# Kernel optimization log

Hardware: AMD Instinct MI355X
Metric: run time of the kernel (lower is better)

## Reference

```python
import jax, jax.numpy as jnp
import numpy as np

NEG_SLOPE = 0.2
EPS = 1e-16

N_NODES = 10000
N_EDGES = 80000
F_IN = 128
HID = 300
H1 = 5  # first_heads
H3 = 3  # out_head
N_CLASSES = 40


def gat_conv(x, edge_index, W, att_src, att_dst, bias, heads, out_ch, concat):
    """PyG-style GATConv (v1 attention), eval mode (no dropout).

    x: [N, F_in]; edge_index: [2, E] (row 0 = source, row 1 = target),
    self-loops already included. W: [F_in, heads*out_ch];
    att_src/att_dst: [heads, out_ch].
    """
    N = x.shape[0]
    h = (x @ W).reshape(N, heads, out_ch)            # [N, H, C]
    a_src = jnp.einsum('nhc,hc->nh', h, att_src)     # [N, H]
    a_dst = jnp.einsum('nhc,hc->nh', h, att_dst)     # [N, H]
    src, dst = edge_index[0], edge_index[1]
    e = jax.nn.leaky_relu(a_src[src] + a_dst[dst], NEG_SLOPE)  # [E, H]
    # segment softmax over incoming edges of each target node
    m = jax.ops.segment_max(e, dst, num_segments=N)  # [N, H]
    ex = jnp.exp(e - m[dst])
    s = jax.ops.segment_sum(ex, dst, num_segments=N)
    alpha = ex / (s[dst] + EPS)                      # [E, H]
    msg = h[src] * alpha[:, :, None]                 # [E, H, C]
    out = jax.ops.segment_sum(msg, dst, num_segments=N)  # [N, H, C]
    if concat:
        out = out.reshape(N, heads * out_ch)
    else:
        out = out.mean(axis=1)
    return out + bias


def setup_inputs() -> dict:
    key = jax.random.key(0)
    ks = jax.random.split(key, 12)
    glorot = lambda k, shape: jax.random.normal(k, shape, jnp.float32) * np.sqrt(
        2.0 / (shape[0] + shape[-1]))
    x = jax.random.normal(ks[0], (N_NODES, F_IN), jnp.float32)
    edge_index = jax.random.randint(ks[1], (2, N_EDGES), 0, N_NODES, jnp.int64)
    return {
        'x': x,
        'edge_index': edge_index,
        'W1': glorot(ks[2], (F_IN, H1 * HID)),
        'as1': glorot(ks[3], (H1, HID)),
        'ad1': glorot(ks[4], (H1, HID)),
        'b1': jnp.zeros((H1 * HID,), jnp.float32),
        'W2': glorot(ks[5], (H1 * HID, H1 * HID)),
        'as2': glorot(ks[6], (H1, HID)),
        'ad2': glorot(ks[7], (H1, HID)),
        'b2': jnp.zeros((H1 * HID,), jnp.float32),
        'W3': glorot(ks[8], (H1 * HID, H3 * N_CLASSES)),
        'as3': glorot(ks[9], (H3, N_CLASSES)),
        'ad3': glorot(ks[10], (H3, N_CLASSES)),
        'b3': jnp.zeros((N_CLASSES,), jnp.float32),
    }


def reference(x, edge_index, W1, as1, ad1, b1, W2, as2, ad2, b2, W3, as3, ad3, b3):
    N = x.shape[0]
    # PyG GATConv adds self-loops by default
    loops = jnp.arange(N, dtype=edge_index.dtype)
    ei = jnp.concatenate([edge_index, jnp.stack([loops, loops])], axis=1)
    # dropout layers are identity in eval mode
    h = gat_conv(x, ei, W1, as1, ad1, b1, H1, HID, True)
    h = jax.nn.elu(h)
    h2 = gat_conv(h, ei, W2, as2, ad2, b2, H1, HID, True)
    h = jax.nn.elu(h + h2)
    h = gat_conv(h, ei, W3, as3, ad3, b3, H3, N_CLASSES, False)  # [N, n_cls]
    pooled = h.sum(axis=0, keepdims=True)                        # [1, n_cls]
    return (pooled, jax.nn.log_softmax(pooled, axis=1))
```

## Files before the change

kernel.cpp:

```cpp
#include <hip/hip_runtime.h>
#include <hip/hip_bf16.h>
#include <math.h>

#define NN       10000
#define F_IN     128
#define HID      300
#define H1       5
#define H3       3
#define NCLS     40
#define HC1      (H1*HID)
#define KPAD     1536
#define HS12     304
#define NL12     1520
#define HS3      48
#define NL3      144
#define LD3      160
#define NEG_SLOPE 0.2f
#define EPSV     1e-16f

typedef __attribute__((ext_vector_type(8))) short bf16x8;
typedef __attribute__((ext_vector_type(8))) unsigned short u16x8;
typedef __attribute__((ext_vector_type(4))) float f32x4;

__device__ inline unsigned short f2bf(float f) {
  unsigned int u = __builtin_bit_cast(unsigned int, f);
  unsigned int r = (u + 0x7FFFu + ((u >> 16) & 1u)) >> 16;
  return (unsigned short)r;
}
__device__ inline float bf2f(unsigned short s) {
  unsigned int u = ((unsigned int)s) << 16;
  return __builtin_bit_cast(float, u);
}

__device__ __forceinline__ void gl2lds16(const unsigned short* g, unsigned short* l) {
  __builtin_amdgcn_global_load_lds(
      (const __attribute__((address_space(1))) unsigned int*)(const void*)g,
      (__attribute__((address_space(3))) unsigned int*)(void*)l, 16, 0, 0);
}

__global__ void k_count(const int* __restrict__ ei, int* __restrict__ counts,
                        int E0, int Etot) {
  int e = blockIdx.x * 256 + threadIdx.x;
  if (e >= Etot) return;
  int dst = (e < E0) ? ei[E0 + e] : (e - E0);
  atomicAdd(&counts[dst], 1);
}

__global__ __launch_bounds__(256) void k_scan(const int* __restrict__ counts,
                                              int* __restrict__ offsets,
                                              int* __restrict__ cursor,
                                              int N, int Etot) {
  __shared__ int sh[256];
  const int CH = 40;
  int t = threadIdx.x;
  int base = t * CH;
  int s = 0;
  for (int i = 0; i < CH; i++) {
    int idx = base + i;
    if (idx < N) s += counts[idx];
  }
  sh[t] = s;
  __syncthreads();
  for (int d = 1; d < 256; d <<= 1) {
    int v = (t >= d) ? sh[t - d] : 0;
    __syncthreads();
    sh[t] += v;
    __syncthreads();
  }
  int run = sh[t] - s;
  for (int i = 0; i < CH; i++) {
    int idx = base + i;
    if (idx < N) {
      offsets[idx] = run;
      cursor[idx] = run;
      run += counts[idx];
    }
  }
  if (t == 0) offsets[N] = Etot;
}

__global__ void k_scatter(const int* __restrict__ ei, int* __restrict__ cursor,
                          int* __restrict__ csr_src, int E0, int Etot) {
  int e = blockIdx.x * 256 + threadIdx.x;
  if (e >= Etot) return;
  int src, dst;
  if (e < E0) { src = ei[e]; dst = ei[E0 + e]; }
  else        { src = dst = e - E0; }
  int pos = atomicAdd(&cursor[dst], 1);
  csr_src[pos] = src;
}

__global__ void k_cvt(const float* __restrict__ in, unsigned short* __restrict__ out,
                      int R, int C, int Cpad) {
  long long idx = (long long)blockIdx.x * 256 + threadIdx.x;
  if (idx >= (long long)R * Cpad) return;
  int r = (int)(idx / Cpad), c = (int)(idx - (long long)r * Cpad);
  out[idx] = (c < C) ? f2bf(in[(size_t)r * C + c]) : 0;
}

__global__ void k_attpad3(const float* __restrict__ as1, const float* __restrict__ ad1,
                          const float* __restrict__ as2, const float* __restrict__ ad2,
                          const float* __restrict__ as3, const float* __restrict__ ad3,
                          float* __restrict__ ps1, float* __restrict__ pd1,
                          float* __restrict__ ps2, float* __restrict__ pd2,
                          float* __restrict__ ps3, float* __restrict__ pd3) {
  int i = blockIdx.x * 256 + threadIdx.x;
  if (i < KPAD) {
    int h = i / HS12, cin = i - h * HS12;
    bool live = (h < H1) && (cin < HID);
    int o = live ? (h * HID + cin) : 0;
    ps1[i] = live ? as1[o] : 0.f;
    pd1[i] = live ? ad1[o] : 0.f;
    ps2[i] = live ? as2[o] : 0.f;
    pd2[i] = live ? ad2[o] : 0.f;
  }
  if (i < LD3) {
    int h = i / HS3, cin = i - h * HS3;
    bool live = (h < H3) && (cin < NCLS);
    ps3[i] = live ? as3[h * NCLS + cin] : 0.f;
    pd3[i] = live ? ad3[h * NCLS + cin] : 0.f;
  }
}

__global__ __launch_bounds__(256) void k_cvtT3(
    const float* __restrict__ W1, const float* __restrict__ W2,
    const float* __restrict__ W3,
    unsigned short* __restrict__ o1, unsigned short* __restrict__ o2,
    unsigned short* __restrict__ o3) {
  const float* in; unsigned short* out;
  int K, Nm, kC, kS, Kp, nC, nS, Nmp;
  if (blockIdx.z == 0) {
    in = W1; out = o1; K = F_IN; Nm = HC1; kC = F_IN; kS = F_IN; Kp = F_IN;
    nC = HID; nS = HS12; Nmp = NL12;
  } else if (blockIdx.z == 1) {
    in = W2; out = o2; K = HC1; Nm = HC1; kC = HID; kS = HS12; Kp = KPAD;
    nC = HID; nS = HS12; Nmp = NL12;
  } else {
    in = W3; out = o3; K = HC1; Nm = H3 * NCLS; kC = HID; kS = HS12; Kp = KPAD;
    nC = NCLS; nS = HS3; Nmp = NL3;
  }
  int k0 = blockIdx.y * 64, n0 = blockIdx.x * 64;
  if (k0 >= Kp || n0 >= Nmp) return;
  __shared__ float tile[64][65];
  int c = threadIdx.x & 63, r = threadIdx.x >> 6;
  for (int rr = r; rr < 64; rr += 4) {
    int kp = k0 + rr;
    int np = n0 + c;
    float v = 0.f;
    if (kp < Kp && np < Nmp) {
      int ck = kp % kS, bk = kp / kS;
      int cn = np % nS, bn_ = np / nS;
      int ko = bk * kC + ck, no = bn_ * nC + cn;
      if (ck < kC && ko < K && cn < nC && no < Nm) v = in[(size_t)ko * Nm + no];
    }
    tile[rr][c] = v;
  }
  __syncthreads();
  for (int rr = r; rr < 64; rr += 4) {
    int np = n0 + rr, kp = k0 + c;
    if (np < Nmp && kp < Kp) out[(size_t)np * Kp + kp] = f2bf(tile[c][rr]);
  }
}

#define BM 256
#define BN 128
#define BK 64

__global__ __launch_bounds__(512) void gemm_mfma(
    const unsigned short* __restrict__ A,
    const unsigned short* __restrict__ Bt,
    unsigned short* __restrict__ Cbf,
    int M, int Kpad, int Nmat, int ldc, int klen, int nT,
    float* __restrict__ Cacc) {
  __shared__ unsigned short As[BM * BK];
  __shared__ unsigned short Bs[BN * BK];
  int tid = threadIdx.x;
  int lane = tid & 63, wid = tid >> 6;
  int wm = wid >> 1, wn = wid & 1;
  int bid = blockIdx.x;
  int slot = bid & 7, idx = bid >> 3;
  int nTi = idx % nT, mg = idx / nT;
  int bm = (slot + 8 * mg) * BM, bn = nTi * BN;
  int quad = lane >> 4, l16 = lane & 15;
  int kq = quad * 8;
  int koff = blockIdx.y * klen;

  int ar0 = min(bm + 32 * wid + l16, M - 1);
  int ar1 = min(bm + 32 * wid + 16 + l16, M - 1);
  int br0 = min(bn + 16 * wid + l16, Nmat - 1);
  const unsigned short* gA0 = A + (size_t)ar0 * Kpad + kq;
  const unsigned short* gA1 = A + (size_t)ar1 * Kpad + kq;
  const unsigned short* gB0 = Bt + (size_t)br0 * Kpad + kq;
  unsigned short* lA = As + 4 * wid * 512;
  unsigned short* lB = Bs + 2 * wid * 512;

  f32x4 acc[4][4] = {};

  for (int kt = koff; kt < koff + klen; kt += BK) {
    gl2lds16(gA0 + kt,      lA);
    gl2lds16(gA0 + kt + 32, lA + 512);
    gl2lds16(gA1 + kt,      lA + 1024);
    gl2lds16(gA1 + kt + 32, lA + 1536);
    gl2lds16(gB0 + kt,      lB);
    gl2lds16(gB0 + kt + 32, lB + 512);
    __syncthreads();
#pragma unroll
    for (int kh = 0; kh < 2; kh++) {
      bf16x8 af[4], bfr[4];
#pragma unroll
      for (int i = 0; i < 4; i++) {
        af[i]  = *(const bf16x8*)(As + ((wm * 4 + i) * 2 + kh) * 512 + lane * 8);
        bfr[i] = *(const bf16x8*)(Bs + ((wn * 4 + i) * 2 + kh) * 512 + lane * 8);
      }
#pragma unroll
      for (int i = 0; i < 4; i++)
#pragma unroll
        for (int j = 0; j < 4; j++)
          acc[i][j] = __builtin_amdgcn_mfma_f32_16x16x32_bf16(af[i], bfr[j], acc[i][j], 0, 0, 0);
    }
    __syncthreads();
  }

#pragma unroll
  for (int i = 0; i < 4; i++) {
    int rowb = bm + wm * 64 + i * 16 + quad * 4;
#pragma unroll
    for (int j = 0; j < 4; j++) {
      int col = bn + wn * 64 + j * 16 + l16;
      if (col < ldc) {
        bool live = col < Nmat;
        if (Cacc) {
#pragma unroll
          for (int r = 0; r < 4; r++) {
            int row = rowb + r;
            if (live && row < M) atomicAdd(&Cacc[(size_t)row * ldc + col], acc[i][j][r]);
          }
        } else {
#pragma unroll
          for (int r = 0; r < 4; r++) {
            int row = rowb + r;
            if (row < M) Cbf[(size_t)row * ldc + col] = live ? f2bf(acc[i][j][r]) : 0;
          }
        }
      }
    }
  }
}

__global__ void k_att(unsigned short* __restrict__ hfeat, int ldh,
                      const float* __restrict__ attp_s,
                      const float* __restrict__ attp_d,
                      float* __restrict__ asrc, float* __restrict__ adst,
                      int H, int HS,
                      const float* __restrict__ Cacc, int Nlive) {
  int n = blockIdx.x, t = threadIdx.x;
  __shared__ float s_ps[8], s_pd[8];
  if (t < 8) { s_ps[t] = 0.f; s_pd[t] = 0.f; }
  __syncthreads();
  int col0 = t * 8;
  if (col0 < ldh) {
    int hj = col0 / HS;
    float ps = 0.f, pd = 0.f;
    if (Cacc) {
      const float4* p = (const float4*)(Cacc + (size_t)n * ldh + col0);
      float4 f0 = p[0], f1 = p[1];
      float fv[8] = {f0.x, f0.y, f0.z, f0.w, f1.x, f1.y, f1.z, f1.w};
      u16x8 st;
#pragma unroll
      for (int j = 0; j < 8; j++) {
        bool live = (col0 + j) < Nlive;
        float v = live ? fv[j] : 0.f;
        st[j] = live ? f2bf(v) : 0;
        ps += v * attp_s[col0 + j];
        pd += v * attp_d[col0 + j];
      }
      *(u16x8*)(hfeat + (size_t)n * ldh + col0) = st;
    } else {
      u16x8 rv = *(const u16x8*)(hfeat + (size_t)n * ldh + col0);
#pragma unroll
      for (int j = 0; j < 8; j++) {
        float v = bf2f(rv[j]);
        ps += v * attp_s[col0 + j];
        pd += v * attp_d[col0 + j];
      }
    }
    atomicAdd(&s_ps[hj], ps);
    atomicAdd(&s_pd[hj], pd);
  }
  __syncthreads();
  if (t < H) {
    asrc[(size_t)n * H + t] = s_ps[t];
    adst[(size_t)n * H + t] = s_pd[t];
  }
}

__global__ __launch_bounds__(64) void k_agg(
    const unsigned short* __restrict__ hfeat, int ldh,
    const float* __restrict__ asrc,
    const float* __restrict__ adst,
    const int* __restrict__ csr_src,
    const int* __restrict__ offsets,
    const float* __restrict__ bias,
    const unsigned short* __restrict__ prevbf,
    unsigned short* __restrict__ out_bf,
    const float* __restrict__ b3,
    float* __restrict__ h3,
    int HS, int C, int H, int mode) {
  int n = blockIdx.x;
  int t = threadIdx.x;
  int s0 = offsets[n], s1 = offsets[n + 1];

  __shared__ float s_ad[8], s_pm[64], s_pl[64], s_mx[8], s_rinv[8];
  __shared__ int s_src[64];
  __shared__ float s_alpha[64 * 8];
  __shared__ float s_out[LD3];

  if (t < 8) s_ad[t] = (t < H) ? adst[(size_t)n * H + t] : 0.f;
  __syncthreads();

  int hh = t & 7, sl = t >> 3;
  float m = -1e30f, l = 0.f;
  if (hh < H) {
    float ad = s_ad[hh];
    for (int p = s0 + sl; p < s1; p += 8) {
      float v = asrc[csr_src[p] * H + hh] + ad;
      v = v > 0.f ? v : NEG_SLOPE * v;
      if (v > m) { l = l * expf(m - v) + 1.f; m = v; }
      else       { l += expf(v - m); }
    }
  }
  s_pm[t] = m; s_pl[t] = l;
  __syncthreads();
  if (t < 8) {
    float M2 = -1e30f, L2 = 0.f;
    for (int k = 0; k < 8; k++) {
      float mk = s_pm[t + 8 * k], lk = s_pl[t + 8 * k];
      if (mk > M2) { L2 = L2 * expf(M2 - mk) + lk; M2 = mk; }
      else         { L2 += lk * expf(mk - M2); }
    }
    s_mx[t] = M2;
    s_rinv[t] = 1.f / (L2 + EPSV);
  }
  __syncthreads();

  int col0 = blockIdx.y * 512 + t * 8;
  bool active = col0 < ldh;
  int hj = active ? (col0 / HS) : 0;
  int cbase = col0 - hj * HS;
  float acc[8] = {};

  for (int base = s0; base < s1; base += 64) {
    int chunk = min(64, s1 - base);
    if (t < chunk) {
      int srcn = csr_src[base + t];
      s_src[t] = srcn;
      const float* ar = asrc + (size_t)srcn * H;
#pragma unroll
      for (int h = 0; h < 8; h++) {
        float a = 0.f;
        if (h < H) {
          float v = ar[h] + s_ad[h];
          v = v > 0.f ? v : NEG_SLOPE * v;
          a = expf(v - s_mx[h]) * s_rinv[h];
        }
        s_alpha[t * 8 + h] = a;
      }
    }
    __syncthreads();
    if (active) {
      const unsigned short* hb = hfeat + col0;
      u16x8 rv0 = {}, rv1 = {};
      if (chunk > 0) rv0 = *(const u16x8*)(hb + (size_t)s_src[0] * ldh);
      if (chunk > 1) rv1 = *(const u16x8*)(hb + (size_t)s_src[1] * ldh);
      int e = 0;
      for (; e + 2 <= chunk; e += 2) {
        u16x8 c0 = rv0, c1 = rv1;
        if (e + 2 < chunk) rv0 = *(const u16x8*)(hb + (size_t)s_src[e + 2] * ldh);
        if (e + 3 < chunk) rv1 = *(const u16x8*)(hb + (size_t)s_src[e + 3] * ldh);
        float a0 = s_alpha[e * 8 + hj];
        float a1 = s_alpha[(e + 1) * 8 + hj];
#pragma unroll
        for (int j = 0; j < 8; j++) {
          acc[j] += a0 * bf2f(c0[j]);
          acc[j] += a1 * bf2f(c1[j]);
        }
      }
      if (e < chunk) {
        float a0 = s_alpha[e * 8 + hj];
#pragma unroll
        for (int j = 0; j < 8; j++) acc[j] += a0 * bf2f(rv0[j]);
      }
    }
    __syncthreads();
  }

  if (mode == 2) {
    if (active) {
#pragma unroll
      for (int j = 0; j < 8; j++) s_out[col0 + j] = acc[j];
    }
    __syncthreads();
    if (t < NCLS)
      h3[(size_t)n * NCLS + t] =
          (s_out[t] + s_out[HS + t] + s_out[2 * HS + t]) * (1.f / 3.f) + b3[t];
    return;
  }

  if (!active) return;
#pragma unroll
  for (int j = 0; j < 8; j++) {
    int cin = cbase + j;
    bool live = (hj < H) && (cin < C);
    float v = 0.f;
    if (live) {
      v = acc[j] + bias[hj * C + cin];
      if (mode == 1) v += bf2f(prevbf[(size_t)n * ldh + col0 + j]);
      v = v > 0.f ? v : (expf(v) - 1.f);
    }
    out_bf[(size_t)n * ldh + col0 + j] = live ? f2bf(v) : 0;
  }
}

__global__ void k_pool(const float* __restrict__ h3, float* __restrict__ pooled,
                       int N) {
  int col = threadIdx.x;
  if (col >= NCLS) return;
  int row = blockIdx.x * 4 + threadIdx.y;
  int stride = gridDim.x * 4;
  float acc = 0.f;
  for (int r = row; r < N; r += stride) acc += h3[(size_t)r * NCLS + col];
  atomicAdd(&pooled[col], acc);
}

__global__ __launch_bounds__(64) void k_final(const float* __restrict__ pooled,
                                              float* __restrict__ out) {
  int t = threadIdx.x;
  float v = (t < NCLS) ? pooled[t] : -INFINITY;
  float m = v;
  for (int o = 32; o > 0; o >>= 1) m = fmaxf(m, __shfl_xor(m, o));
  float ex = (t < NCLS) ? expf(v - m) : 0.f;
  float s = ex;
  for (int o = 32; o > 0; o >>= 1) s += __shfl_xor(s, o);
  float lse = m + logf(s);
  if (t < NCLS) {
    out[t] = v;
    out[NCLS + t] = v - lse;
  }
}

extern "C" void kernel_launch(void* const* d_in, const int* in_sizes, int n_in,
                              void* d_out, int out_size, void* d_ws, size_t ws_size,
                              hipStream_t stream) {
  const float* x   = (const float*)d_in[0];
  const int*   ei  = (const int*)d_in[1];
  const float* W1  = (const float*)d_in[2];
  const float* as1 = (const float*)d_in[3];
  const float* ad1 = (const float*)d_in[4];
  const float* b1  = (const float*)d_in[5];
  const float* W2  = (const float*)d_in[6];
  const float* as2 = (const float*)d_in[7];
  const float* ad2 = (const float*)d_in[8];
  const float* b2  = (const float*)d_in[9];
  const float* W3  = (const float*)d_in[10];
  const float* as3 = (const float*)d_in[11];
  const float* ad3 = (const float*)d_in[12];
  const float* b3  = (const float*)d_in[13];
  float* out = (float*)d_out;

  const int N = NN;
  const int E0 = in_sizes[1] / 2;
  const int Etot = E0 + N;
  const int mT = (N + BM - 1) / BM;

  float* f = (float*)d_ws;
  float* asrc   = f;
  float* adst   = asrc + (size_t)N * H1;
  float* pooled = adst + (size_t)N * H1;
  float* h3     = pooled + 64;
  float* attps1 = h3 + (size_t)N * NCLS;
  float* attpd1 = attps1 + KPAD;
  float* attps2 = attpd1 + KPAD;
  float* attpd2 = attps2 + KPAD;
  float* attps3 = attpd2 + KPAD;
  float* attpd3 = attps3 + LD3;
  float* Cacc   = attpd3 + LD3;
  int* counts  = (int*)(Cacc + (size_t)N * LD3);
  int* offsets = counts + N;
  int* cursor  = offsets + N + 1;
  int* csr_src = cursor + N;
  uintptr_t pp = (uintptr_t)(csr_src + Etot);
  pp = (pp + 15) & ~(uintptr_t)15;
  unsigned short* hfbf  = (unsigned short*)pp;
  unsigned short* abf   = hfbf + (size_t)N * KPAD;
  unsigned short* btbf1 = abf + (size_t)N * KPAD;
  unsigned short* btbf2 = btbf1 + (size_t)NL12 * F_IN;
  unsigned short* btbf3 = btbf2 + (size_t)NL12 * KPAD;

  hipMemsetAsync(counts, 0, (size_t)N * sizeof(int), stream);
  hipMemsetAsync(pooled, 0, 64 * sizeof(float), stream);
  hipMemsetAsync(Cacc, 0, (size_t)N * LD3 * sizeof(float), stream);

  k_count<<<(Etot + 255) / 256, 256, 0, stream>>>(ei, counts, E0, Etot);
  k_scan<<<1, 256, 0, stream>>>(counts, offsets, cursor, N, Etot);
  k_scatter<<<(Etot + 255) / 256, 256, 0, stream>>>(ei, cursor, csr_src, E0, Etot);
  {
    dim3 tg((NL12 + 63) / 64, (KPAD + 63) / 64, 3);
    k_cvtT3<<<tg, 256, 0, stream>>>(W1, W2, W3, btbf1, btbf2, btbf3);
  }
  k_attpad3<<<(KPAD + 255) / 256, 256, 0, stream>>>(as1, ad1, as2, ad2, as3, ad3,
                                                    attps1, attpd1, attps2, attpd2,
                                                    attps3, attpd3);

  {
    k_cvt<<<((long long)N * F_IN + 255) / 256, 256, 0, stream>>>(x, abf, N, F_IN, F_IN);
    int nT = (NL12 + BN - 1) / BN;
    gemm_mfma<<<dim3(nT * mT, 1), 512, 0, stream>>>(abf, btbf1, hfbf, N, F_IN, NL12,
                                                    KPAD, F_IN, nT, nullptr);
    k_att<<<N, 192, 0, stream>>>(hfbf, KPAD, attps1, attpd1, asrc, adst, H1, HS12,
                                 nullptr, 0);
    k_agg<<<dim3(N, 3), 64, 0, stream>>>(hfbf, KPAD, asrc, adst, csr_src, offsets,
                                         b1, nullptr, abf, nullptr, nullptr,
                                         HS12, HID, H1, 0);
  }

  {
    int nT = (NL12 + BN - 1) / BN;
    gemm_mfma<<<dim3(nT * mT, 1), 512, 0, stream>>>(abf, btbf2, hfbf, N, KPAD, NL12,
                                                    KPAD, KPAD, nT, nullptr);
    k_att<<<N, 192, 0, stream>>>(hfbf, KPAD, attps2, attpd2, asrc, adst, H1, HS12,
                                 nullptr, 0);
    k_agg<<<dim3(N, 3), 64, 0, stream>>>(hfbf, KPAD, asrc, adst, csr_src, offsets,
                                         b2, abf, abf, nullptr, nullptr,
                                         HS12, HID, H1, 1);
  }

  {
    int nT = (LD3 + BN - 1) / BN;
    gemm_mfma<<<dim3(nT * mT, 4), 512, 0, stream>>>(abf, btbf3, nullptr, N, KPAD, NL3,
                                                    LD3, KPAD / 4, nT, Cacc);
    k_att<<<N, 64, 0, stream>>>(hfbf, LD3, attps3, attpd3, asrc, adst, H3, HS3,
                                Cacc, NL3);
    k_agg<<<dim3(N, 1), 64, 0, stream>>>(hfbf, LD3, asrc, adst, csr_src, offsets,
                                         nullptr, nullptr, nullptr, b3, h3,
                                         HS3, NCLS, H3, 2);
  }

  k_pool<<<64, dim3(64, 4), 0, stream>>>(h3, pooled, N);
  k_final<<<1, 64, 0, stream>>>(pooled, out);
}
```

Before: 523.3 us.

## Merge prep kernels, coalesce memsets, widen aggregation blocks, deepen gather prefetch

Folds the attention-vector padding kernel into the weight transpose/convert kernel as an extra grid z-slice, and reorders the workspace so three memsets become one contiguous memset. The layer 1/2 aggregation now uses one 192-thread block per node instead of three 64-thread blocks per node, so the edge-softmax statistics are computed once per node rather than three times. The feature gather loop is unrolled to four edges with four prefetched rows to raise memory-level parallelism. The costs are fewer blocks in the aggregation grid and more registers per thread.

Result: slower. 613.5 us (+17.2%).

```diff
diff --git a/kernel.cpp b/kernel.cpp
--- a/kernel.cpp
+++ b/kernel.cpp
@@ -98,35 +98,38 @@
   out[idx] = (c < C) ? f2bf(in[(size_t)r * C + c]) : 0;
 }
 
-__global__ void k_attpad3(const float* __restrict__ as1, const float* __restrict__ ad1,
-                          const float* __restrict__ as2, const float* __restrict__ ad2,
-                          const float* __restrict__ as3, const float* __restrict__ ad3,
-                          float* __restrict__ ps1, float* __restrict__ pd1,
-                          float* __restrict__ ps2, float* __restrict__ pd2,
-                          float* __restrict__ ps3, float* __restrict__ pd3) {
-  int i = blockIdx.x * 256 + threadIdx.x;
-  if (i < KPAD) {
-    int h = i / HS12, cin = i - h * HS12;
-    bool live = (h < H1) && (cin < HID);
-    int o = live ? (h * HID + cin) : 0;
-    ps1[i] = live ? as1[o] : 0.f;
-    pd1[i] = live ? ad1[o] : 0.f;
-    ps2[i] = live ? as2[o] : 0.f;
-    pd2[i] = live ? ad2[o] : 0.f;
-  }
-  if (i < LD3) {
-    int h = i / HS3, cin = i - h * HS3;
-    bool live = (h < H3) && (cin < NCLS);
-    ps3[i] = live ? as3[h * NCLS + cin] : 0.f;
-    pd3[i] = live ? ad3[h * NCLS + cin] : 0.f;
-  }
-}
-
-__global__ __launch_bounds__(256) void k_cvtT3(
+__global__ __launch_bounds__(256) void k_prep(
     const float* __restrict__ W1, const float* __restrict__ W2,
     const float* __restrict__ W3,
     unsigned short* __restrict__ o1, unsigned short* __restrict__ o2,
-    unsigned short* __restrict__ o3) {
+    unsigned short* __restrict__ o3,
+    const float* __restrict__ as1, const float* __restrict__ ad1,
+    const float* __restrict__ as2, const float* __restrict__ ad2,
+    const float* __restrict__ as3, const float* __restrict__ ad3,
+    float* __restrict__ ps1, float* __restrict__ pd1,
+    float* __restrict__ ps2, float* __restrict__ pd2,
+    float* __restrict__ ps3, float* __restrict__ pd3) {
+  if (blockIdx.z == 3) {
+    int gi = blockIdx.y * gridDim.x + blockIdx.x;
+    if (gi >= 6) return;
+    int i = gi * 256 + threadIdx.x;
+    if (i < KPAD) {
+      int h = i / HS12, cin = i - h * HS12;
+      bool live = (h < H1) && (cin < HID);
+      int o = live ? (h * HID + cin) : 0;
+      ps1[i] = live ? as1[o] : 0.f;
+      pd1[i] = live ? ad1[o] : 0.f;
+      ps2[i] = live ? as2[o] : 0.f;
+      pd2[i] = live ? ad2[o] : 0.f;
+    }
+    if (i < LD3) {
+      int h = i / HS3, cin = i - h * HS3;
+      bool live = (h < H3) && (cin < NCLS);
+      ps3[i] = live ? as3[h * NCLS + cin] : 0.f;
+      pd3[i] = live ? ad3[h * NCLS + cin] : 0.f;
+    }
+    return;
+  }
   const float* in; unsigned short* out;
   int K, Nm, kC, kS, Kp, nC, nS, Nmp;
   if (blockIdx.z == 0) {
@@ -294,7 +297,7 @@
   }
 }
 
-__global__ __launch_bounds__(64) void k_agg(
+__global__ void k_agg(
     const unsigned short* __restrict__ hfeat, int ldh,
     const float* __restrict__ asrc,
     const float* __restrict__ adst,
@@ -308,9 +311,10 @@
     int HS, int C, int H, int mode) {
   int n = blockIdx.x;
   int t = threadIdx.x;
+  int nthr = blockDim.x;
   int s0 = offsets[n], s1 = offsets[n + 1];
 
-  __shared__ float s_ad[8], s_pm[64], s_pl[64], s_mx[8], s_rinv[8];
+  __shared__ float s_ad[8], s_pm[192], s_pl[192], s_mx[8], s_rinv[8];
   __shared__ int s_src[64];
   __shared__ float s_alpha[64 * 8];
   __shared__ float s_out[LD3];
@@ -318,11 +322,12 @@
   if (t < 8) s_ad[t] = (t < H) ? adst[(size_t)n * H + t] : 0.f;
   __syncthreads();
 
+  int slices = nthr >> 3;
   int hh = t & 7, sl = t >> 3;
   float m = -1e30f, l = 0.f;
   if (hh < H) {
     float ad = s_ad[hh];
-    for (int p = s0 + sl; p < s1; p += 8) {
+    for (int p = s0 + sl; p < s1; p += slices) {
       float v = asrc[csr_src[p] * H + hh] + ad;
       v = v > 0.f ? v : NEG_SLOPE * v;
       if (v > m) { l = l * expf(m - v) + 1.f; m = v; }
@@ -333,7 +338,7 @@
   __syncthreads();
   if (t < 8) {
     float M2 = -1e30f, L2 = 0.f;
-    for (int k = 0; k < 8; k++) {
+    for (int k = 0; k < slices; k++) {
       float mk = s_pm[t + 8 * k], lk = s_pl[t + 8 * k];
       if (mk > M2) { L2 = L2 * expf(M2 - mk) + lk; M2 = mk; }
       else         { L2 += lk * expf(mk - M2); }
@@ -343,7 +348,7 @@
   }
   __syncthreads();
 
-  int col0 = blockIdx.y * 512 + t * 8;
+  int col0 = t * 8;
   bool active = col0 < ldh;
   int hj = active ? (col0 / HS) : 0;
   int cbase = col0 - hj * HS;
@@ -369,26 +374,30 @@
     __syncthreads();
     if (active) {
       const unsigned short* hb = hfeat + col0;
-      u16x8 rv0 = {}, rv1 = {};
-      if (chunk > 0) rv0 = *(const u16x8*)(hb + (size_t)s_src[0] * ldh);
-      if (chunk > 1) rv1 = *(const u16x8*)(hb + (size_t)s_src[1] * ldh);
+      u16x8 r[4] = {};
+#pragma unroll
+      for (int q = 0; q < 4; q++)
+        if (q < chunk) r[q] = *(const u16x8*)(hb + (size_t)s_src[q] * ldh);
       int e = 0;
-      for (; e + 2 <= chunk; e += 2) {
-        u16x8 c0 = rv0, c1 = rv1;
-        if (e + 2 < chunk) rv0 = *(const u16x8*)(hb + (size_t)s_src[e + 2] * ldh);
-        if (e + 3 < chunk) rv1 = *(const u16x8*)(hb + (size_t)s_src[e + 3] * ldh);
+      for (; e + 4 <= chunk; e += 4) {
+        u16x8 c0 = r[0], c1 = r[1], c2 = r[2], c3 = r[3];
+#pragma unroll
+        for (int q = 0; q < 4; q++)
+          if (e + 4 + q < chunk) r[q] = *(const u16x8*)(hb + (size_t)s_src[e + 4 + q] * ldh);
         float a0 = s_alpha[e * 8 + hj];
         float a1 = s_alpha[(e + 1) * 8 + hj];
+        float a2 = s_alpha[(e + 2) * 8 + hj];
+        float a3 = s_alpha[(e + 3) * 8 + hj];
 #pragma unroll
         for (int j = 0; j < 8; j++) {
-          acc[j] += a0 * bf2f(c0[j]);
-          acc[j] += a1 * bf2f(c1[j]);
+          acc[j] += a0 * bf2f(c0[j]) + a1 * bf2f(c1[j]);
+          acc[j] += a2 * bf2f(c2[j]) + a3 * bf2f(c3[j]);
         }
       }
-      if (e < chunk) {
-        float a0 = s_alpha[e * 8 + hj];
-#pragma unroll
-        for (int j = 0; j < 8; j++) acc[j] += a0 * bf2f(rv0[j]);
+      for (int q = 0; e + q < chunk; q++) {
+        float a = s_alpha[(e + q) * 8 + hj];
+#pragma unroll
+        for (int j = 0; j < 8; j++) acc[j] += a * bf2f(r[q][j]);
       }
     }
     __syncthreads();
@@ -476,16 +485,16 @@
   float* asrc   = f;
   float* adst   = asrc + (size_t)N * H1;
   float* pooled = adst + (size_t)N * H1;
-  float* h3     = pooled + 64;
+  float* Cacc   = pooled + 64;
+  int* counts  = (int*)(Cacc + (size_t)N * LD3);
+  float* h3     = (float*)(counts + N);
   float* attps1 = h3 + (size_t)N * NCLS;
   float* attpd1 = attps1 + KPAD;
   float* attps2 = attpd1 + KPAD;
   float* attpd2 = attps2 + KPAD;
   float* attps3 = attpd2 + KPAD;
   float* attpd3 = attps3 + LD3;
-  float* Cacc   = attpd3 + LD3;
-  int* counts  = (int*)(Cacc + (size_t)N * LD3);
-  int* offsets = counts + N;
+  int* offsets = (int*)(attpd3 + LD3);
   int* cursor  = offsets + N + 1;
   int* csr_src = cursor + N;
   uintptr_t pp = (uintptr_t)(csr_src + Etot);
@@ -496,20 +505,18 @@
   unsigned short* btbf2 = btbf1 + (size_t)NL12 * F_IN;
   unsigned short* btbf3 = btbf2 + (size_t)NL12 * KPAD;
 
-  hipMemsetAsync(counts, 0, (size_t)N * sizeof(int), stream);
-  hipMemsetAsync(pooled, 0, 64 * sizeof(float), stream);
-  hipMemsetAsync(Cacc, 0, (size_t)N * LD3 * sizeof(float), stream);
+  hipMemsetAsync(pooled, 0, (64 + (size_t)N * LD3) * sizeof(float) + N * sizeof(int),
+                 stream);
 
   k_count<<<(Etot + 255) / 256, 256, 0, stream>>>(ei, counts, E0, Etot);
   k_scan<<<1, 256, 0, stream>>>(counts, offsets, cursor, N, Etot);
   k_scatter<<<(Etot + 255) / 256, 256, 0, stream>>>(ei, cursor, csr_src, E0, Etot);
   {
-    dim3 tg((NL12 + 63) / 64, (KPAD + 63) / 64, 3);
-    k_cvtT3<<<tg, 256, 0, stream>>>(W1, W2, W3, btbf1, btbf2, btbf3);
-  }
-  k_attpad3<<<(KPAD + 255) / 256, 256, 0, stream>>>(as1, ad1, as2, ad2, as3, ad3,
-                                                    attps1, attpd1, attps2, attpd2,
-                                                    attps3, attpd3);
+    dim3 tg((NL12 + 63) / 64, (KPAD + 63) / 64, 4);
+    k_prep<<<tg, 256, 0, stream>>>(W1, W2, W3, btbf1, btbf2, btbf3,
+                                   as1, ad1, as2, ad2, as3, ad3,
+                                   attps1, attpd1, attps2, attpd2, attps3, attpd3);
+  }
 
   {
     k_cvt<<<((long long)N * F_IN + 255) / 256, 256, 0, stream>>>(x, abf, N, F_IN, F_IN);
@@ -518,9 +525,9 @@
                                                     KPAD, F_IN, nT, nullptr);
     k_att<<<N, 192, 0, stream>>>(hfbf, KPAD, attps1, attpd1, asrc, adst, H1, HS12,
                                  nullptr, 0);
-    k_agg<<<dim3(N, 3), 64, 0, stream>>>(hfbf, KPAD, asrc, adst, csr_src, offsets,
-                                         b1, nullptr, abf, nullptr, nullptr,
-                                         HS12, HID, H1, 0);
+    k_agg<<<N, 192, 0, stream>>>(hfbf, KPAD, asrc, adst, csr_src, offsets,
+                                 b1, nullptr, abf, nullptr, nullptr,
+                                 HS12, HID, H1, 0);
   }
 
   {
@@ -529,9 +536,9 @@
                                                     KPAD, KPAD, nT, nullptr);
     k_att<<<N, 192, 0, stream>>>(hfbf, KPAD, attps2, attpd2, asrc, adst, H1, HS12,
                                  nullptr, 0);
-    k_agg<<<dim3(N, 3), 64, 0, stream>>>(hfbf, KPAD, asrc, adst, csr_src, offsets,
-                                         b2, abf, abf, nullptr, nullptr,
-                                         HS12, HID, H1, 1);
+    k_agg<<<N, 192, 0, stream>>>(hfbf, KPAD, asrc, adst, csr_src, offsets,
+                                 b2, abf, abf, nullptr, nullptr,
+                                 HS12, HID, H1, 1);
   }
 
   {
@@ -540,9 +547,9 @@
                                                     LD3, KPAD / 4, nT, Cacc);
     k_att<<<N, 64, 0, stream>>>(hfbf, LD3, attps3, attpd3, asrc, adst, H3, HS3,
                                 Cacc, NL3);
-    k_agg<<<dim3(N, 1), 64, 0, stream>>>(hfbf, LD3, asrc, adst, csr_src, offsets,
-                                         nullptr, nullptr, nullptr, b3, h3,
-                                         HS3, NCLS, H3, 2);
+    k_agg<<<N, 64, 0, stream>>>(hfbf, LD3, asrc, adst, csr_src, offsets,
+                                nullptr, nullptr, nullptr, b3, h3,
+                                HS3, NCLS, H3, 2);
   }
 
   k_pool<<<64, dim3(64, 4), 0, stream>>>(h3, pooled, N);
```
